# Optimization experiments

Measured on AMD Instinct MI355X. Metric: run time of the kernel, lower is better.

The kernel has to match this reference:

```python
import jax, jax.numpy as jnp
import numpy as np
import math

B, T, I, H, W = 4096, 24, 128, 512, 32


def setup_inputs() -> dict:
    key = jax.random.key(0)
    ks = jax.random.split(key, 32)
    stdv = 1.0 / math.sqrt(H)
    u = lambda k, shape: jax.random.uniform(k, shape, jnp.float32, -stdv, stdv)
    inp = {
        'x_input': jax.random.normal(ks[0], (B, T, I), jnp.float32),
        'x_weather': jax.random.normal(ks[1], (B, T, W), jnp.float32),
        'w_rx': u(ks[2], (H, I)), 'w_rh': u(ks[3], (H, H)), 'w_re': u(ks[4], (H, H)), 'b_r': u(ks[5], (H, 1)),
        'w_zx': u(ks[6], (H, I)), 'w_zh': u(ks[7], (H, H)), 'w_ze': u(ks[8], (H, H)), 'b_z': u(ks[9], (H, 1)),
        'w_hx': u(ks[10], (H, I)), 'w_hh': u(ks[11], (H, H)), 'b_h': u(ks[12], (H, 1)),
        'w_d': u(ks[13], (H, I)), 'w_w': u(ks[14], (H, I)), 'w_m': u(ks[15], (H, I)),
        'w_t': u(ks[16], (H, H)), 'w_e': u(ks[17], (H, W)), 'b_e': u(ks[18], (H, 1)),
    }
    return inp


def _shift_days(x, k):
    # x: [B,T,I]; prepend k zero-days (history unavailable for first k days)
    pad = jnp.zeros((k,) + x.shape[1:], x.dtype)
    return jnp.concatenate([pad, x[:-k]], axis=0)


def _forward(x_input, x_weather, w_rx, w_rh, w_re, b_r, w_zx, w_zh, w_ze, b_z,
             w_hx, w_hh, b_h, w_d, w_w, w_m, w_t, w_e, b_e):
    h_d = _shift_days(x_input, 1)
    h_w = _shift_days(x_input, 7)
    h_m = _shift_days(x_input, 30)
    # precompute all input-only projections: [B,T,H]
    pre_o = (jnp.einsum('bti,hi->bth', h_d, w_d)
             + jnp.einsum('bti,hi->bth', h_w, w_w)
             + jnp.einsum('bti,hi->bth', h_m, w_m))
    e = jax.nn.sigmoid(jnp.einsum('btw,hw->bth', x_weather, w_e) + b_e[:, 0])
    pre_r = jnp.einsum('bti,hi->bth', x_input, w_rx) + jnp.einsum('bth,gh->btg', e, w_re) + b_r[:, 0]
    pre_z = jnp.einsum('bti,hi->bth', x_input, w_zx) + jnp.einsum('bth,gh->btg', e, w_ze) + b_z[:, 0]
    pre_h = jnp.einsum('bti,hi->bth', x_input, w_hx) + b_h[:, 0]

    def step(h_t, xs_t):
        po, pr, pz, ph = xs_t  # each [B,H]
        h_o = jax.nn.sigmoid(po + h_t @ w_t.T)
        r = jax.nn.sigmoid(pr + h_o @ w_rh.T)
        z = jax.nn.sigmoid(pz + h_o @ w_zh.T)
        h_tilde = jnp.tanh(ph + (r * h_o) @ w_hh.T)
        h_next = (1.0 - z) * h_o + z * h_tilde
        return h_next, h_next

    h0 = jnp.zeros((x_input.shape[0], w_t.shape[0]), x_input.dtype)
    xs = tuple(a.transpose(1, 0, 2) for a in (pre_o, pre_r, pre_z, pre_h))  # [T,B,H]
    _, hs = jax.lax.scan(step, h0, xs)
    return hs.transpose(1, 0, 2)  # [B,T,H]


def reference(x_input, x_weather, w_rx, w_rh, w_re, b_r, w_zx, w_zh, w_ze, b_z,
              w_hx, w_hh, b_h, w_d, w_w, w_m, w_t, w_e, b_e):
    return _forward(x_input, x_weather, w_rx, w_rh, w_re, b_r, w_zx, w_zh, w_ze, b_z,
                    w_hx, w_hh, b_h, w_d, w_w, w_m, w_t, w_e, b_e)
```

## Files before the change

### kernel.cpp

```cpp
#include <hip/hip_runtime.h>
#include <stdint.h>

#define Bsz 4096
#define Tsz 24
#define Isz 128
#define Hsz 512
#define Wsz 32
#define Msz (Bsz * Tsz)

typedef __attribute__((ext_vector_type(8))) short short8;
typedef __attribute__((ext_vector_type(4))) float f32x4;
typedef unsigned short u16;

__device__ __forceinline__ float bf2f(u16 u) {
    union { unsigned int i; float f; } v; v.i = ((unsigned int)u) << 16; return v.f;
}
__device__ __forceinline__ u16 f2bf(float f) {
    union { float f; unsigned int i; } v; v.f = f;
    unsigned int r = v.i + 0x7fffu + ((v.i >> 16) & 1u);
    return (u16)(r >> 16);
}
__device__ __forceinline__ float sigm(float x) { return 1.0f / (1.0f + expf(-x)); }

__device__ __forceinline__ f32x4 MF(short8 a, short8 b, f32x4 c) {
    return __builtin_amdgcn_mfma_f32_16x16x32_bf16(a, b, c, 0, 0, 0);
}
__device__ __forceinline__ short8 ntload8(const u16* p) {
    return __builtin_nontemporal_load((const short8*)p);
}

#define GLOAD_LDS16(SRC, DST) \
    __builtin_amdgcn_global_load_lds( \
        (__attribute__((address_space(1))) void*)(SRC), \
        (__attribute__((address_space(3))) void*)(DST), 16, 0, 0)

__global__ __launch_bounds__(256) void convert_big(
    const float* __restrict__ src, u16* __restrict__ dst, int n)
{
    int i = (blockIdx.x * 256 + threadIdx.x) * 4;
    if (i + 4 <= n) {
        float4 v = *(const float4*)(src + i);
        dst[i + 0] = f2bf(v.x); dst[i + 1] = f2bf(v.y);
        dst[i + 2] = f2bf(v.z); dst[i + 3] = f2bf(v.w);
    }
}

struct ConvDesc { const float* src; u16* dst; int n; };
struct ConvTab { ConvDesc d[13]; };

__global__ __launch_bounds__(256) void convert_many(ConvTab tab)
{
    ConvDesc cd = tab.d[blockIdx.y];
    for (int i = (blockIdx.x * 256 + threadIdx.x) * 4; i < cd.n;
         i += gridDim.x * 256 * 4) {
        float4 v = *(const float4*)(cd.src + i);
        cd.dst[i + 0] = f2bf(v.x); cd.dst[i + 1] = f2bf(v.y);
        cd.dst[i + 2] = f2bf(v.z); cd.dst[i + 3] = f2bf(v.w);
    }
}

struct Seg { const u16* A; int astr; int shift; const u16* W; int wstr; int nkb; };

__device__ __forceinline__ void stage_half(
    u16* ldsT, const u16* gbase, int rstr, int rvf,
    const u16* zerobuf, int wid, int lane)
{
#pragma unroll
    for (int q = 0; q < 4; ++q) {
        int c   = wid * 4 + q;
        int lin = c * 64 + lane;
        int row = lin >> 3;
        int gc  = lin & 7;
        const u16* src = (row >= rvf)
            ? (gbase + (long)row * rstr + ((gc ^ (row & 7)) << 3))
            : zerobuf;
        GLOAD_LDS16(src, ldsT + c * 512);
    }
}

__device__ __forceinline__ void stage_step(
    const Seg* segs, int nseg, int kb, u16* ldsA, u16* ldsB,
    int m0, int n0, const u16* zerobuf, int wid, int lane)
{
    Seg s = segs[0];
    int kloc = kb;
    if (nseg > 1 && kloc >= s.nkb) {
        kloc -= s.nkb; s = segs[1];
        if (nseg > 2 && kloc >= s.nkb) { kloc -= s.nkb; s = segs[2]; }
    }
    int base_row = m0 + s.shift;
    int rvf = base_row < 0 ? -base_row : 0;
    stage_half(ldsA, s.A + (long)base_row * s.astr + kloc * 64, s.astr, rvf,
               zerobuf, wid, lane);
    stage_half(ldsB, s.W + (long)n0 * s.wstr + kloc * 64, s.wstr, 0,
               zerobuf, wid, lane);
}

__device__ __forceinline__ void compute_tile(
    f32x4 acc[4][4], const u16* Ab, const u16* Bb, int wr, int wc, int lane)
{
    const int l15 = lane & 15;
    const int hi = lane >> 4;
#pragma unroll
    for (int ks = 0; ks < 2; ++ks) {
        int kg = ks * 4 + hi;
        short8 a[4], b[4];
#pragma unroll
        for (int am = 0; am < 4; ++am) {
            int row = wr * 64 + am * 16 + l15;
            a[am] = *(const short8*)(Ab + row * 64 + ((kg ^ (row & 7)) << 3));
        }
#pragma unroll
        for (int bn = 0; bn < 4; ++bn) {
            int row = wc * 64 + bn * 16 + l15;
            b[bn] = *(const short8*)(Bb + row * 64 + ((kg ^ (row & 7)) << 3));
        }
#pragma unroll
        for (int am = 0; am < 4; ++am)
#pragma unroll
            for (int bn = 0; bn < 4; ++bn)
                acc[am][bn] = MF(a[am], b[bn], acc[am][bn]);
    }
}

#define GEMM_CORE(SEGS, NSEG, M0, N0W)                                          \
    __shared__ u16 lds[2][2][128 * 64];                                         \
    const int lane = threadIdx.x & 63;                                          \
    const int wid  = threadIdx.x >> 6;                                          \
    const int wr = wid >> 1, wc = wid & 1;                                      \
    f32x4 acc[4][4];                                                            \
    _Pragma("unroll") for (int i_ = 0; i_ < 4; ++i_)                            \
    _Pragma("unroll") for (int j_ = 0; j_ < 4; ++j_)                            \
        acc[i_][j_] = f32x4{0, 0, 0, 0};                                        \
    int nkb = 0;                                                                \
    for (int s_ = 0; s_ < (NSEG); ++s_) nkb += (SEGS)[s_].nkb;                  \
    stage_step((SEGS), (NSEG), 0, lds[0][0], lds[0][1], (M0), (N0W),            \
               zerobuf, wid, lane);                                             \
    int cur = 0;                                                                \
    for (int kb = 0; kb < nkb; ++kb) {                                          \
        __syncthreads();                                                        \
        if (kb + 1 < nkb)                                                       \
            stage_step((SEGS), (NSEG), kb + 1, lds[cur ^ 1][0],                 \
                       lds[cur ^ 1][1], (M0), (N0W), zerobuf, wid, lane);       \
        compute_tile(acc, lds[cur][0], lds[cur][1], wr, wc, lane);              \
        cur ^= 1;                                                               \
    }

__global__ __launch_bounds__(256) void ekernel(
    const u16* __restrict__ xw, const u16* __restrict__ w_e,
    const float* __restrict__ b_e, u16* __restrict__ eout)
{
    const int lane = threadIdx.x & 63;
    const int wid  = threadIdx.x >> 6;
    const int m0 = blockIdx.x * 64 + (wid >> 1) * 32;
    const int n0 = blockIdx.y * 64 + (wid & 1) * 32;
    f32x4 acc[2][2];
    acc[0][0] = f32x4{0,0,0,0}; acc[0][1] = f32x4{0,0,0,0};
    acc[1][0] = f32x4{0,0,0,0}; acc[1][1] = f32x4{0,0,0,0};
    const int l15 = lane & 15;
    const int klane = (lane >> 4) * 8;
    short8 b0 = *(const short8*)(w_e + (n0 + l15) * Wsz + klane);
    short8 b1 = *(const short8*)(w_e + (n0 + 16 + l15) * Wsz + klane);
#pragma unroll
    for (int am = 0; am < 2; ++am) {
        short8 a = *(const short8*)(xw + (long)(m0 + am * 16 + l15) * Wsz + klane);
        acc[am][0] = MF(a, b0, acc[am][0]);
        acc[am][1] = MF(a, b1, acc[am][1]);
    }
    const int col = lane & 15;
    const int r0 = (lane >> 4) * 4;
#pragma unroll
    for (int am = 0; am < 2; ++am)
#pragma unroll
        for (int bn = 0; bn < 2; ++bn)
#pragma unroll
            for (int i = 0; i < 4; ++i) {
                long row = m0 + am * 16 + r0 + i;
                int g = n0 + bn * 16 + col;
                eout[row * Hsz + g] = f2bf(sigm(acc[am][bn][i] + b_e[g]));
            }
}

__global__ __launch_bounds__(256, 2) void prepass_kernel(
    const u16* __restrict__ x, const u16* __restrict__ e,
    const u16* __restrict__ w_d, const u16* __restrict__ w_w,
    const u16* __restrict__ w_m, const u16* __restrict__ w_rx,
    const u16* __restrict__ w_re, const u16* __restrict__ w_zx,
    const u16* __restrict__ w_ze, const u16* __restrict__ w_hx,
    const float* __restrict__ b_r, const float* __restrict__ b_z,
    const float* __restrict__ b_h,
    const u16* __restrict__ zerobuf, u16* __restrict__ prep)
{
    const int m0 = blockIdx.x * 128;
    const int y = blockIdx.y;
    const int group = y >> 2;
    const int nin = (y & 3) * 128;
    Seg segs[3];
    int nseg;
    const float* bias = nullptr;
    if (group == 0) {
        segs[0] = { x, Isz, -1 * Tsz,  w_d, Isz, Isz / 64 };
        segs[1] = { x, Isz, -7 * Tsz,  w_w, Isz, Isz / 64 };
        segs[2] = { x, Isz, -30 * Tsz, w_m, Isz, Isz / 64 };
        nseg = 3;
    } else if (group == 1) {
        segs[0] = { x, Isz, 0, w_rx, Isz, Isz / 64 };
        segs[1] = { e, Hsz, 0, w_re, Hsz, Hsz / 64 };
        nseg = 2; bias = b_r;
    } else if (group == 2) {
        segs[0] = { x, Isz, 0, w_zx, Isz, Isz / 64 };
        segs[1] = { e, Hsz, 0, w_ze, Hsz, Hsz / 64 };
        nseg = 2; bias = b_z;
    } else {
        segs[0] = { x, Isz, 0, w_hx, Isz, Isz / 64 };
        nseg = 1; bias = b_h;
    }
    GEMM_CORE(segs, nseg, m0, nin)
    const int l15 = lane & 15, hi4v = (lane >> 4) * 4;
#pragma unroll
    for (int am = 0; am < 4; ++am)
#pragma unroll
        for (int bn = 0; bn < 4; ++bn) {
            int colH = nin + wc * 64 + bn * 16 + l15;
            float bv = bias ? bias[colH] : 0.0f;
            int wv = colH >> 5, ntv = (colH >> 4) & 1, l15v = colH & 15;
#pragma unroll
            for (int i = 0; i < 4; ++i) {
                long m = m0 + wr * 64 + am * 16 + hi4v + i;
                int b = (int)(m / Tsz), t = (int)(m % Tsz);
                int bblk = b >> 4, rowin = b & 15;
                int hiv = rowin >> 2, iv = rowin & 3;
                long idx = (((long)(bblk * Tsz + t) * 4 + group) * 16 + wv) * 512
                           + (hiv * 16 + l15v) * 8 + ntv * 4 + iv;
                prep[idx] = f2bf(acc[am][bn][i] + bv);
            }
        }
}

#define SROW 528

__device__ __forceinline__ int swz(int row, int col) {
    return row * SROW + ((((col >> 3) ^ (row & 7)) << 3) | (col & 7));
}

__device__ __forceinline__ void stage_chunk(
    const u16* __restrict__ Wm, int c, u16* buf, int wave, int lane)
{
    int s1 = wave * 128 + lane;
    int s2 = s1 + 64;
    int p1 = s1 >> 3, g1 = (s1 & 7) ^ (p1 & 7);
    int p2 = s2 >> 3, g2 = (s2 & 7) ^ (p2 & 7);
    GLOAD_LDS16(Wm + (long)(2 * p1 + (g1 >> 2)) * 512 + c * 32 + (g1 & 3) * 8,
                buf + wave * 1024);
    GLOAD_LDS16(Wm + (long)(2 * p2 + (g2 >> 2)) * 512 + c * 32 + (g2 & 3) * 8,
                buf + wave * 1024 + 512);
}

__device__ __forceinline__ void wpass_staged(
    f32x4 acc[2], const u16* aS, const u16* __restrict__ Wm,
    u16* wbuf0, u16* wbuf1, int n0, int l15, int hi, int wave, int lane)
{
    const int rx = l15 & 7;
    const u16* ap = aS + l15 * SROW;
    const int bo0 = (wave * 128 + (l15 >> 1) * 8
                     + ((hi + 4 * (l15 & 1)) ^ (l15 >> 1))) * 8;
    stage_chunk(Wm, 0, wbuf0, wave, lane);
#pragma unroll 1
    for (int c = 0; c < 16; ++c) {
        __syncthreads();
        u16* cur = (c & 1) ? wbuf1 : wbuf0;
        u16* nxt = (c & 1) ? wbuf0 : wbuf1;
        if (c < 15) stage_chunk(Wm, c + 1, nxt, wave, lane);
        short8 b0 = *(const short8*)(cur + bo0);
        short8 b1 = *(const short8*)(cur + bo0 + 512);
        short8 a = *(const short8*)(ap + (((c * 4 + hi) ^ rx) << 3));
        acc[0] = MF(a, b0, acc[0]);
        acc[1] = MF(a, b1, acc[1]);
    }
}

#define FOR_FRAG \
    _Pragma("unroll") for (int nt2 = 0; nt2 < 2; ++nt2) \
    _Pragma("unroll") for (int i = 0; i < 4; ++i)

__global__ __launch_bounds__(1024, 4) void rnn_kernel(
    const u16* __restrict__ prep, const u16* __restrict__ w_t_,
    const u16* __restrict__ w_rh, const u16* __restrict__ w_zh,
    const u16* __restrict__ w_hh, float* __restrict__ out)
{
    __shared__ __align__(16) u16 hS[16 * SROW];
    __shared__ __align__(16) u16 hoS[16 * SROW];
    __shared__ __align__(16) u16 rhS[16 * SROW];
    __shared__ __align__(16) u16 wbuf0[16 * 1024];
    __shared__ __align__(16) u16 wbuf1[16 * 1024];
    const int tid = threadIdx.x;
    const int lane = tid & 63;
    const int wave = tid >> 6;
    const int l15 = lane & 15, hi = lane >> 4;
    const int n0 = wave * 32;
    const long b0 = (long)blockIdx.x * 16;

    for (int i = tid * 8; i < 16 * SROW; i += 1024 * 8)
        *(short8*)(hS + i) = (short8)0;
    __syncthreads();

    const u16* pbase = prep + (long)blockIdx.x * (Tsz * 4 * 8192)
                       + wave * 512 + lane * 8;

#pragma unroll 1
    for (int t = 0; t < Tsz; ++t) {
        const u16* pt = pbase + (long)t * 4 * 8192;
        short8 po = ntload8(pt);

        f32x4 accO[2];
        accO[0] = f32x4{0,0,0,0}; accO[1] = f32x4{0,0,0,0};
        wpass_staged(accO, hS, w_t_, wbuf0, wbuf1, n0, l15, hi, wave, lane);
        float hov[2][4];
        FOR_FRAG {
            float v = sigm(accO[nt2][i] + bf2f((u16)po[nt2 * 4 + i]));
            hov[nt2][i] = v;
            hoS[swz(hi * 4 + i, n0 + nt2 * 16 + l15)] = f2bf(v);
        }

        short8 pr = ntload8(pt + 8192);
        short8 pz = ntload8(pt + 2 * 8192);
        f32x4 accR[2];
        accR[0] = f32x4{0,0,0,0}; accR[1] = f32x4{0,0,0,0};
        wpass_staged(accR, hoS, w_rh, wbuf0, wbuf1, n0, l15, hi, wave, lane);
        f32x4 accZ[2];
        accZ[0] = f32x4{0,0,0,0}; accZ[1] = f32x4{0,0,0,0};
        wpass_staged(accZ, hoS, w_zh, wbuf0, wbuf1, n0, l15, hi, wave, lane);
        float zv[2][4];
        FOR_FRAG {
            zv[nt2][i] = sigm(accZ[nt2][i] + bf2f((u16)pz[nt2 * 4 + i]));
            float rv = sigm(accR[nt2][i] + bf2f((u16)pr[nt2 * 4 + i]));
            rhS[swz(hi * 4 + i, n0 + nt2 * 16 + l15)] = f2bf(rv * hov[nt2][i]);
        }

        short8 ph = ntload8(pt + 3 * 8192);
        f32x4 accH[2];
        accH[0] = f32x4{0,0,0,0}; accH[1] = f32x4{0,0,0,0};
        wpass_staged(accH, rhS, w_hh, wbuf0, wbuf1, n0, l15, hi, wave, lane);
        FOR_FRAG {
            int row = hi * 4 + i, col = n0 + nt2 * 16 + l15;
            float htl = tanhf(accH[nt2][i] + bf2f((u16)ph[nt2 * 4 + i]));
            float z = zv[nt2][i];
            float hn = (1.0f - z) * hov[nt2][i] + z * htl;
            __builtin_nontemporal_store(
                hn, &out[((b0 + row) * Tsz + t) * (long)Hsz + col]);
            hS[swz(row, col)] = f2bf(hn);
        }
        __syncthreads();
    }
}

extern "C" void kernel_launch(void* const* d_in, const int* in_sizes, int n_in,
                              void* d_out, int out_size, void* d_ws, size_t ws_size,
                              hipStream_t stream) {
    const float* x_f    = (const float*)d_in[0];
    const float* xw_f   = (const float*)d_in[1];
    const float* w_rx_f = (const float*)d_in[2];
    const float* w_rh_f = (const float*)d_in[3];
    const float* w_re_f = (const float*)d_in[4];
    const float* b_r    = (const float*)d_in[5];
    const float* w_zx_f = (const float*)d_in[6];
    const float* w_zh_f = (const float*)d_in[7];
    const float* w_ze_f = (const float*)d_in[8];
    const float* b_z    = (const float*)d_in[9];
    const float* w_hx_f = (const float*)d_in[10];
    const float* w_hh_f = (const float*)d_in[11];
    const float* b_h    = (const float*)d_in[12];
    const float* w_d_f  = (const float*)d_in[13];
    const float* w_w_f  = (const float*)d_in[14];
    const float* w_m_f  = (const float*)d_in[15];
    const float* w_t_f  = (const float*)d_in[16];
    const float* w_e_f  = (const float*)d_in[17];
    const float* b_e    = (const float*)d_in[18];
    float* out = (float*)d_out;

    char* ws = (char*)d_ws;
    size_t off = 0;
    auto alloc = [&](size_t bytes) {
        size_t o = off; off = (off + bytes + 255) & ~(size_t)255; return o;
    };
    const size_t nx  = (size_t)Msz * Isz;
    const size_t nxw = (size_t)Msz * Wsz;

    u16* x_bf  = (u16*)(ws + alloc(nx * 2));
    u16* xw_bf = (u16*)(ws + alloc(nxw * 2));
    u16* w_rx  = (u16*)(ws + alloc(Hsz * Isz * 2));
    u16* w_rh  = (u16*)(ws + alloc(Hsz * Hsz * 2));
    u16* w_re  = (u16*)(ws + alloc(Hsz * Hsz * 2));
    u16* w_zx  = (u16*)(ws + alloc(Hsz * Isz * 2));
    u16* w_zh  = (u16*)(ws + alloc(Hsz * Hsz * 2));
    u16* w_ze  = (u16*)(ws + alloc(Hsz * Hsz * 2));
    u16* w_hx  = (u16*)(ws + alloc(Hsz * Isz * 2));
    u16* w_hh  = (u16*)(ws + alloc(Hsz * Hsz * 2));
    u16* w_d   = (u16*)(ws + alloc(Hsz * Isz * 2));
    u16* w_w   = (u16*)(ws + alloc(Hsz * Isz * 2));
    u16* w_m   = (u16*)(ws + alloc(Hsz * Isz * 2));
    u16* w_t   = (u16*)(ws + alloc(Hsz * Hsz * 2));
    u16* w_e   = (u16*)(ws + alloc(Hsz * Wsz * 2));
    u16* e_bf  = (u16*)(ws + alloc((size_t)Msz * Hsz * 2));
    u16* prep  = (u16*)(ws + alloc((size_t)Msz * 2048 * 2));
    u16* zerobuf = (u16*)(ws + alloc(256));

    convert_big<<<(int)(nx / 1024), 256, 0, stream>>>(x_f, x_bf, (int)nx);
    convert_big<<<(int)(nxw / 1024), 256, 0, stream>>>(xw_f, xw_bf, (int)nxw);
    ConvTab tab;
    tab.d[0]  = { w_rx_f, w_rx, Hsz * Isz };
    tab.d[1]  = { w_rh_f, w_rh, Hsz * Hsz };
    tab.d[2]  = { w_re_f, w_re, Hsz * Hsz };
    tab.d[3]  = { w_zx_f, w_zx, Hsz * Isz };
    tab.d[4]  = { w_zh_f, w_zh, Hsz * Hsz };
    tab.d[5]  = { w_ze_f, w_ze, Hsz * Hsz };
    tab.d[6]  = { w_hx_f, w_hx, Hsz * Isz };
    tab.d[7]  = { w_hh_f, w_hh, Hsz * Hsz };
    tab.d[8]  = { w_d_f,  w_d,  Hsz * Isz };
    tab.d[9]  = { w_w_f,  w_w,  Hsz * Isz };
    tab.d[10] = { w_m_f,  w_m,  Hsz * Isz };
    tab.d[11] = { w_t_f,  w_t,  Hsz * Hsz };
    tab.d[12] = { w_e_f,  w_e,  Hsz * Wsz };
    convert_many<<<dim3(256, 13), 256, 0, stream>>>(tab);
    hipMemsetAsync(zerobuf, 0, 256, stream);

    ekernel<<<dim3(Msz / 64, Hsz / 64), 256, 0, stream>>>(xw_bf, w_e, b_e, e_bf);

    prepass_kernel<<<dim3(Msz / 128, 16), 256, 0, stream>>>(
        x_bf, e_bf, w_d, w_w, w_m, w_rx, w_re, w_zx, w_ze, w_hx,
        b_r, b_z, b_h, zerobuf, prep);

    rnn_kernel<<<Bsz / 16, 1024, 0, stream>>>(prep, w_t, w_rh, w_zh, w_hh, out);
}
```

Measured before the change: 1.733 ms.

## Stage 64-wide weight chunks and reuse one activation buffer to halve barriers

The weight staging loop now moves two 32-column K slices per stage, which halves the number of chunk iterations and __syncthreads calls per matrix pass. The freed LDS from dropping the separate hoS and rhS buffers pays for the doubled weight buffers. h_o and r*h_o are written back into hS behind extra barriers. This trades fewer barriers for larger LDS staging per block and a few added synchronisation points between phases, which may lower occupancy.

```diff
diff --git a/kernel.cpp b/kernel.cpp
--- a/kernel.cpp
+++ b/kernel.cpp
@@ -243,39 +243,46 @@
     return row * SROW + ((((col >> 3) ^ (row & 7)) << 3) | (col & 7));
 }
 
-__device__ __forceinline__ void stage_chunk(
+__device__ __forceinline__ void stage_chunk64(
     const u16* __restrict__ Wm, int c, u16* buf, int wave, int lane)
 {
     int s1 = wave * 128 + lane;
     int s2 = s1 + 64;
     int p1 = s1 >> 3, g1 = (s1 & 7) ^ (p1 & 7);
     int p2 = s2 >> 3, g2 = (s2 & 7) ^ (p2 & 7);
-    GLOAD_LDS16(Wm + (long)(2 * p1 + (g1 >> 2)) * 512 + c * 32 + (g1 & 3) * 8,
-                buf + wave * 1024);
-    GLOAD_LDS16(Wm + (long)(2 * p2 + (g2 >> 2)) * 512 + c * 32 + (g2 & 3) * 8,
-                buf + wave * 1024 + 512);
+#pragma unroll
+    for (int h = 0; h < 2; ++h) {
+        GLOAD_LDS16(Wm + (long)(2 * p1 + (g1 >> 2)) * 512
+                       + c * 64 + h * 32 + (g1 & 3) * 8,
+                    buf + h * 16384 + wave * 1024);
+        GLOAD_LDS16(Wm + (long)(2 * p2 + (g2 >> 2)) * 512
+                       + c * 64 + h * 32 + (g2 & 3) * 8,
+                    buf + h * 16384 + wave * 1024 + 512);
+    }
 }
 
 __device__ __forceinline__ void wpass_staged(
     f32x4 acc[2], const u16* aS, const u16* __restrict__ Wm,
-    u16* wbuf0, u16* wbuf1, int n0, int l15, int hi, int wave, int lane)
-{
-    const int rx = l15 & 7;
+    u16* wbuf0, u16* wbuf1, int bo0, int rx, int l15, int hi,
+    int wave, int lane)
+{
     const u16* ap = aS + l15 * SROW;
-    const int bo0 = (wave * 128 + (l15 >> 1) * 8
-                     + ((hi + 4 * (l15 & 1)) ^ (l15 >> 1))) * 8;
-    stage_chunk(Wm, 0, wbuf0, wave, lane);
+    stage_chunk64(Wm, 0, wbuf0, wave, lane);
 #pragma unroll 1
-    for (int c = 0; c < 16; ++c) {
+    for (int c = 0; c < 8; ++c) {
         __syncthreads();
         u16* cur = (c & 1) ? wbuf1 : wbuf0;
         u16* nxt = (c & 1) ? wbuf0 : wbuf1;
-        if (c < 15) stage_chunk(Wm, c + 1, nxt, wave, lane);
-        short8 b0 = *(const short8*)(cur + bo0);
-        short8 b1 = *(const short8*)(cur + bo0 + 512);
-        short8 a = *(const short8*)(ap + (((c * 4 + hi) ^ rx) << 3));
-        acc[0] = MF(a, b0, acc[0]);
-        acc[1] = MF(a, b1, acc[1]);
+        if (c < 7) stage_chunk64(Wm, c + 1, nxt, wave, lane);
+#pragma unroll
+        for (int kk = 0; kk < 2; ++kk) {
+            short8 b0 = *(const short8*)(cur + kk * 16384 + bo0);
+            short8 b1 = *(const short8*)(cur + kk * 16384 + bo0 + 512);
+            short8 a = *(const short8*)(
+                ap + ((((c * 2 + kk) * 4 + hi) ^ rx) << 3));
+            acc[0] = MF(a, b0, acc[0]);
+            acc[1] = MF(a, b1, acc[1]);
+        }
     }
 }
 
@@ -289,16 +296,17 @@
     const u16* __restrict__ w_hh, float* __restrict__ out)
 {
     __shared__ __align__(16) u16 hS[16 * SROW];
-    __shared__ __align__(16) u16 hoS[16 * SROW];
-    __shared__ __align__(16) u16 rhS[16 * SROW];
-    __shared__ __align__(16) u16 wbuf0[16 * 1024];
-    __shared__ __align__(16) u16 wbuf1[16 * 1024];
+    __shared__ __align__(16) u16 wbuf0[32 * 1024];
+    __shared__ __align__(16) u16 wbuf1[32 * 1024];
     const int tid = threadIdx.x;
     const int lane = tid & 63;
     const int wave = tid >> 6;
     const int l15 = lane & 15, hi = lane >> 4;
+    const int rx = l15 & 7;
     const int n0 = wave * 32;
     const long b0 = (long)blockIdx.x * 16;
+    const int bo0 = (wave * 128 + (l15 >> 1) * 8
+                     + ((hi + 4 * (l15 & 1)) ^ (l15 >> 1))) * 8;
 
     for (int i = tid * 8; i < 16 * SROW; i += 1024 * 8)
         *(short8*)(hS + i) = (short8)0;
@@ -314,33 +322,41 @@
 
         f32x4 accO[2];
         accO[0] = f32x4{0,0,0,0}; accO[1] = f32x4{0,0,0,0};
-        wpass_staged(accO, hS, w_t_, wbuf0, wbuf1, n0, l15, hi, wave, lane);
+        wpass_staged(accO, hS, w_t_, wbuf0, wbuf1, bo0, rx, l15, hi,
+                     wave, lane);
         float hov[2][4];
         FOR_FRAG {
             float v = sigm(accO[nt2][i] + bf2f((u16)po[nt2 * 4 + i]));
             hov[nt2][i] = v;
-            hoS[swz(hi * 4 + i, n0 + nt2 * 16 + l15)] = f2bf(v);
-        }
+        }
+        __syncthreads();
+        FOR_FRAG hS[swz(hi * 4 + i, n0 + nt2 * 16 + l15)] = f2bf(hov[nt2][i]);
 
         short8 pr = ntload8(pt + 8192);
         short8 pz = ntload8(pt + 2 * 8192);
         f32x4 accR[2];
         accR[0] = f32x4{0,0,0,0}; accR[1] = f32x4{0,0,0,0};
-        wpass_staged(accR, hoS, w_rh, wbuf0, wbuf1, n0, l15, hi, wave, lane);
+        wpass_staged(accR, hS, w_rh, wbuf0, wbuf1, bo0, rx, l15, hi,
+                     wave, lane);
         f32x4 accZ[2];
         accZ[0] = f32x4{0,0,0,0}; accZ[1] = f32x4{0,0,0,0};
-        wpass_staged(accZ, hoS, w_zh, wbuf0, wbuf1, n0, l15, hi, wave, lane);
-        float zv[2][4];
+        wpass_staged(accZ, hS, w_zh, wbuf0, wbuf1, bo0, rx, l15, hi,
+                     wave, lane);
+        float zv[2][4], rhv[2][4];
         FOR_FRAG {
             zv[nt2][i] = sigm(accZ[nt2][i] + bf2f((u16)pz[nt2 * 4 + i]));
             float rv = sigm(accR[nt2][i] + bf2f((u16)pr[nt2 * 4 + i]));
-            rhS[swz(hi * 4 + i, n0 + nt2 * 16 + l15)] = f2bf(rv * hov[nt2][i]);
-        }
+            rhv[nt2][i] = rv * hov[nt2][i];
+        }
+        __syncthreads();
+        FOR_FRAG hS[swz(hi * 4 + i, n0 + nt2 * 16 + l15)] = f2bf(rhv[nt2][i]);
 
         short8 ph = ntload8(pt + 3 * 8192);
         f32x4 accH[2];
         accH[0] = f32x4{0,0,0,0}; accH[1] = f32x4{0,0,0,0};
-        wpass_staged(accH, rhS, w_hh, wbuf0, wbuf1, n0, l15, hi, wave, lane);
+        wpass_staged(accH, hS, w_hh, wbuf0, wbuf1, bo0, rx, l15, hi,
+                     wave, lane);
+        __syncthreads();
         FOR_FRAG {
             int row = hi * 4 + i, col = n0 + nt2 * 16 + l15;
             float htl = tanhf(accH[nt2][i] + bf2f((u16)ph[nt2 * 4 + i]));
@@ -350,7 +366,6 @@
                 hn, &out[((b0 + row) * Tsz + t) * (long)Hsz + col]);
             hS[swz(row, col)] = f2bf(hn);
         }
-        __syncthreads();
     }
 }
 
```

New measurement: 1.597 ms. -7.8%, faster.
